# Optimization experiments

Measured on AMD Instinct MI355X. Metric: run time of the kernel, lower is better.

The kernel has to match this reference:

```python
import jax, jax.numpy as jnp
import numpy as np

B, N, FIN, FOUT, K, NNZ = 16, 50000, 32, 32, 6, 800000


def setup_inputs() -> dict:
    key = jax.random.key(0)
    k1, k2, k3, k4, k5 = jax.random.split(key, 5)
    x = jax.random.normal(k1, (B, N, FIN), dtype=jnp.float32)
    rows = jax.random.randint(k2, (NNZ,), 0, N, dtype=jnp.int32)
    cols = jax.random.randint(k3, (NNZ,), 0, N, dtype=jnp.int32)
    # values of the already-rescaled Laplacian (2L/lmax - I), scaled to keep the
    # Chebyshev recurrence numerically tame
    vals = jax.random.normal(k4, (NNZ,), dtype=jnp.float32) * 0.05
    W = jax.random.normal(k5, (FIN * K, FOUT), dtype=jnp.float32) * 0.02
    return {"x": x, "rows": rows, "cols": cols, "vals": vals, "W": W}


def reference(x, rows, cols, vals, W):
    # x: [B, N, Fin]
    def spmm(X):  # L @ X via gather + segment-sum scatter; X: [N, D]
        return jax.ops.segment_sum(vals[:, None] * X[cols], rows, num_segments=N)

    # [N, Fin, B] -> [N, Fin*B], matching the TF layout
    x0 = jnp.transpose(x, (1, 2, 0)).reshape(N, FIN * B)
    xs = [x0]
    x1 = spmm(x0)
    xs.append(x1)
    for _ in range(2, K):  # Chebyshev recurrence T_k = 2 L T_{k-1} - T_{k-2}
        x2 = 2.0 * spmm(x1) - x0
        xs.append(x2)
        x0, x1 = x1, x2
    Xk = jnp.stack(xs, axis=0)                       # [K, N, Fin*B]
    Xk = Xk.reshape(K, N, FIN, B)
    Xk = jnp.transpose(Xk, (3, 1, 2, 0))             # [B, N, Fin, K]
    Xk = Xk.reshape(B * N, FIN * K)
    out = Xk @ W                                      # [B*N, Fout]
    return out.reshape(B, N, FOUT)
```

## Files before the change

kernel.cpp:

```cpp
#include <hip/hip_runtime.h>
#include <hip/hip_bf16.h>

#define NND   50000
#define NBATCH 16
#define NFIN  32
#define NFOUT 32
#define NCHEB 6
#define NNZE  800000
#define DDIM  512

typedef __attribute__((ext_vector_type(8))) short    short8;
typedef __attribute__((ext_vector_type(8))) unsigned short u16x8;
typedef __attribute__((ext_vector_type(4))) float    f32x4;
typedef __attribute__((ext_vector_type(2))) float    f32x2;

__device__ __forceinline__ float b2f(unsigned short u) {
  union { unsigned u; float f; } v; v.u = ((unsigned)u) << 16; return v.f;
}
__device__ __forceinline__ unsigned short f2bf(float f) {
  union { float f; unsigned u; } v; v.f = f;
  unsigned r = v.u + 0x7fffu + ((v.u >> 16) & 1u);
  return (unsigned short)(r >> 16);
}
__device__ __forceinline__ unsigned f2fp8(float f) {
  unsigned s = (__float_as_uint(f) >> 24) & 0x80u;
  float af = fminf(fabsf(f), 448.0f);
  unsigned b;
  if (af < 0.015625f) {
    b = (unsigned)__float2int_rn(af * 512.0f);
  } else {
    unsigned u = __float_as_uint(af);
    u += 0x7FFFFu + ((u >> 20) & 1u);
    b = (((u >> 23) - 120u) << 3) | ((u >> 20) & 7u);
    if (b > 0x7Eu) b = 0x7Eu;
  }
  return s | b;
}

__global__ void hist_kernel(const int* __restrict__ rows, int* __restrict__ cnt, int nnz) {
  int e = blockIdx.x * blockDim.x + threadIdx.x;
  if (e < nnz) atomicAdd(&cnt[rows[e]], 1);
}

__global__ __launch_bounds__(1024) void scanA_kernel(const int* __restrict__ cnt,
                                                     int* __restrict__ rowptr,
                                                     int* __restrict__ partials, int n) {
  __shared__ int lds[1024];
  int b = blockIdx.x, tid = threadIdx.x, i = b * 1024 + tid;
  int v = (i < n) ? cnt[i] : 0;
  lds[tid] = v;
  __syncthreads();
  int s = v;
  for (int off = 1; off < 1024; off <<= 1) {
    int t = (tid >= off) ? lds[tid - off] : 0;
    __syncthreads();
    s += t;
    lds[tid] = s;
    __syncthreads();
  }
  if (i < n) rowptr[i] = s - v;
  if (tid == 1023) partials[b] = s;
}

__global__ void scanB_wprep(int* __restrict__ partials, int nb,
                            const float* __restrict__ W, unsigned short* __restrict__ Wfrag) {
  int t = threadIdx.x;
  if (t == 0) {
    int run = 0;
    for (int b = 0; b < nb; ++b) { int x = partials[b]; partials[b] = run; run += x; }
  } else if (t >= 64 && t < 64 + 768) {
    int w = t - 64;
    int frag = w >> 6, lane = w & 63;
    int kk = frag >> 1, h = frag & 1;
    int fo = (lane & 15) + h * 16, kc = (lane >> 4) * 8;
    u16x8 b;
#pragma unroll
    for (int j = 0; j < 8; ++j)
      b[j] = f2bf(W[((size_t)(kc + j) * NCHEB + kk) * NFOUT + fo]);
    *(u16x8*)(Wfrag + (size_t)w * 8) = b;
  }
}

__global__ __launch_bounds__(1024) void scanC_kernel(const int* __restrict__ partials,
                                                     int* __restrict__ rowptr,
                                                     int* __restrict__ cursor, int n) {
  int i = blockIdx.x * 1024 + threadIdx.x;
  if (i < n) {
    int r = rowptr[i] + partials[blockIdx.x];
    rowptr[i] = r;
    cursor[i] = r;
  }
  if (i == n) rowptr[n] = NNZE;
}

__global__ void fill_kernel(const int* __restrict__ rows, const int* __restrict__ cols,
                            const float* __restrict__ vals, int* __restrict__ cursor,
                            long* __restrict__ ecv, int nnz) {
  int e = blockIdx.x * blockDim.x + threadIdx.x;
  if (e < nnz) {
    int r = rows[e];
    int p = atomicAdd(&cursor[r], 1);
    ecv[p] = (long)((unsigned long long)__float_as_uint(vals[e]) << 32 | (unsigned)cols[e]);
  }
}

__global__ __launch_bounds__(256) void cheb_k0_q(const float* __restrict__ x,
                                                 unsigned short* __restrict__ T0,
                                                 char* __restrict__ Tq0) {
  int wave = threadIdx.x >> 6, lane = threadIdx.x & 63;
  int n = blockIdx.x * 4 + wave;
  int kc = (lane >> 4) * 8;
  int b  = lane & 15;

  const float* xp = x + ((size_t)b * NND + n) * NFIN + kc;
  float4 xa = *(const float4*)xp;
  float4 xb = *(const float4*)(xp + 4);
  float tv[8] = {xa.x, xa.y, xa.z, xa.w, xb.x, xb.y, xb.z, xb.w};

  u16x8 tb;
#pragma unroll
  for (int j = 0; j < 8; ++j) tb[j] = f2bf(tv[j]);
  *(u16x8*)(T0 + (size_t)n * DDIM + lane * 8) = tb;

  unsigned lo = f2fp8(tv[0]) | (f2fp8(tv[1]) << 8) | (f2fp8(tv[2]) << 16) | (f2fp8(tv[3]) << 24);
  unsigned hi = f2fp8(tv[4]) | (f2fp8(tv[5]) << 8) | (f2fp8(tv[6]) << 16) | (f2fp8(tv[7]) << 24);
  int2 qq; qq.x = (int)lo; qq.y = (int)hi;
  *(int2*)(Tq0 + (size_t)n * 512 + lane * 8) = qq;
}

__device__ __forceinline__ void gather_q(const char* __restrict__ qbase,
                                         const long* __restrict__ ecv,
                                         int s, int e1, float acc[8]) {
  int e = s;
  for (; e + 8 <= e1; e += 8) {
    long m[8];
#pragma unroll
    for (int q = 0; q < 8; ++q) m[q] = __builtin_nontemporal_load(ecv + e + q);
    int2 d[8];
#pragma unroll
    for (int q = 0; q < 8; ++q) d[q] = *(const int2*)(qbase + (size_t)(int)m[q] * 512);
#pragma unroll
    for (int q = 0; q < 8; ++q) {
      float v = __int_as_float((int)(m[q] >> 32));
      f32x2 f01 = __builtin_amdgcn_cvt_pk_f32_fp8(d[q].x, false);
      f32x2 f23 = __builtin_amdgcn_cvt_pk_f32_fp8(d[q].x, true);
      f32x2 f45 = __builtin_amdgcn_cvt_pk_f32_fp8(d[q].y, false);
      f32x2 f67 = __builtin_amdgcn_cvt_pk_f32_fp8(d[q].y, true);
      acc[0] = fmaf(v, f01.x, acc[0]);
      acc[1] = fmaf(v, f01.y, acc[1]);
      acc[2] = fmaf(v, f23.x, acc[2]);
      acc[3] = fmaf(v, f23.y, acc[3]);
      acc[4] = fmaf(v, f45.x, acc[4]);
      acc[5] = fmaf(v, f45.y, acc[5]);
      acc[6] = fmaf(v, f67.x, acc[6]);
      acc[7] = fmaf(v, f67.y, acc[7]);
    }
  }
  if (e + 4 <= e1) {
    long m[4];
#pragma unroll
    for (int q = 0; q < 4; ++q) m[q] = __builtin_nontemporal_load(ecv + e + q);
    int2 d[4];
#pragma unroll
    for (int q = 0; q < 4; ++q) d[q] = *(const int2*)(qbase + (size_t)(int)m[q] * 512);
#pragma unroll
    for (int q = 0; q < 4; ++q) {
      float v = __int_as_float((int)(m[q] >> 32));
      f32x2 f01 = __builtin_amdgcn_cvt_pk_f32_fp8(d[q].x, false);
      f32x2 f23 = __builtin_amdgcn_cvt_pk_f32_fp8(d[q].x, true);
      f32x2 f45 = __builtin_amdgcn_cvt_pk_f32_fp8(d[q].y, false);
      f32x2 f67 = __builtin_amdgcn_cvt_pk_f32_fp8(d[q].y, true);
      acc[0] = fmaf(v, f01.x, acc[0]);
      acc[1] = fmaf(v, f01.y, acc[1]);
      acc[2] = fmaf(v, f23.x, acc[2]);
      acc[3] = fmaf(v, f23.y, acc[3]);
      acc[4] = fmaf(v, f45.x, acc[4]);
      acc[5] = fmaf(v, f45.y, acc[5]);
      acc[6] = fmaf(v, f67.x, acc[6]);
      acc[7] = fmaf(v, f67.y, acc[7]);
    }
    e += 4;
  }
  for (; e < e1; ++e) {
    long mm = __builtin_nontemporal_load(ecv + e);
    int2 dd = *(const int2*)(qbase + (size_t)(int)mm * 512);
    float v = __int_as_float((int)(mm >> 32));
    f32x2 f01 = __builtin_amdgcn_cvt_pk_f32_fp8(dd.x, false);
    f32x2 f23 = __builtin_amdgcn_cvt_pk_f32_fp8(dd.x, true);
    f32x2 f45 = __builtin_amdgcn_cvt_pk_f32_fp8(dd.y, false);
    f32x2 f67 = __builtin_amdgcn_cvt_pk_f32_fp8(dd.y, true);
    acc[0] = fmaf(v, f01.x, acc[0]);
    acc[1] = fmaf(v, f01.y, acc[1]);
    acc[2] = fmaf(v, f23.x, acc[2]);
    acc[3] = fmaf(v, f23.y, acc[3]);
    acc[4] = fmaf(v, f45.x, acc[4]);
    acc[5] = fmaf(v, f45.y, acc[5]);
    acc[6] = fmaf(v, f67.x, acc[6]);
    acc[7] = fmaf(v, f67.y, acc[7]);
  }
}

__global__ __launch_bounds__(256) void cheb_level_q(const char* __restrict__ Tqprev,
                                                    const unsigned short* __restrict__ Tpp,
                                                    unsigned short* __restrict__ Tdst,
                                                    char* __restrict__ Tqdst,
                                                    const int* __restrict__ rowptr,
                                                    const long* __restrict__ ecv,
                                                    float alpha, float beta) {
  int wave = threadIdx.x >> 6, lane = threadIdx.x & 63;
  int n = blockIdx.x * 4 + wave;
  int s = rowptr[n], e1 = rowptr[n + 1];
  size_t rowoff = (size_t)n * DDIM + lane * 8;

  u16x8 tp2 = {};
  if (beta != 0.f) tp2 = *(const u16x8*)(Tpp + rowoff);

  float acc[8] = {0.f, 0.f, 0.f, 0.f, 0.f, 0.f, 0.f, 0.f};
  gather_q(Tqprev + (size_t)lane * 8, ecv, s, e1, acc);

  float tk[8];
  if (beta != 0.f) {
#pragma unroll
    for (int j = 0; j < 8; ++j) tk[j] = alpha * acc[j] - beta * b2f(tp2[j]);
  } else {
#pragma unroll
    for (int j = 0; j < 8; ++j) tk[j] = alpha * acc[j];
  }

  u16x8 tkb;
#pragma unroll
  for (int j = 0; j < 8; ++j) tkb[j] = f2bf(tk[j]);
  *(u16x8*)(Tdst + rowoff) = tkb;

  unsigned lo = f2fp8(tk[0]) | (f2fp8(tk[1]) << 8) | (f2fp8(tk[2]) << 16) | (f2fp8(tk[3]) << 24);
  unsigned hi = f2fp8(tk[4]) | (f2fp8(tk[5]) << 8) | (f2fp8(tk[6]) << 16) | (f2fp8(tk[7]) << 24);
  int2 qq; qq.x = (int)lo; qq.y = (int)hi;
  *(int2*)(Tqdst + (size_t)n * 512 + lane * 8) = qq;
}

__global__ __launch_bounds__(256) void cheb_level5_epi_q(const char* __restrict__ Tq4,
                                                         const unsigned short* __restrict__ Tall,
                                                         const unsigned short* __restrict__ Wfrag,
                                                         const int* __restrict__ rowptr,
                                                         const long* __restrict__ ecv,
                                                         float* __restrict__ out) {
  int wave = threadIdx.x >> 6, lane = threadIdx.x & 63;
  int n = blockIdx.x * 4 + wave;
  int s = rowptr[n], e1 = rowptr[n + 1];
  size_t rowoff = (size_t)n * DDIM + lane * 8;

  float acc[8] = {0.f, 0.f, 0.f, 0.f, 0.f, 0.f, 0.f, 0.f};
  gather_q(Tq4 + (size_t)lane * 8, ecv, s, e1, acc);

  short8 a[5];
#pragma unroll
  for (int kk = 0; kk < 5; ++kk)
    a[kk] = *(const short8*)(Tall + (size_t)kk * NND * DDIM + rowoff);

  u16x8 tp2 = __builtin_bit_cast(u16x8, a[3]);
  u16x8 t5b;
#pragma unroll
  for (int j = 0; j < 8; ++j) t5b[j] = f2bf(2.f * acc[j] - b2f(tp2[j]));

  int fo = lane & 15;
  f32x4 c0 = {0.f, 0.f, 0.f, 0.f}, c1 = {0.f, 0.f, 0.f, 0.f};
#pragma unroll
  for (int kk = 0; kk < 5; ++kk) {
    short8 B0 = *(const short8*)(Wfrag + ((size_t)(kk * 2 + 0) * 64 + lane) * 8);
    short8 B1 = *(const short8*)(Wfrag + ((size_t)(kk * 2 + 1) * 64 + lane) * 8);
    c0 = __builtin_amdgcn_mfma_f32_16x16x32_bf16(a[kk], B0, c0, 0, 0, 0);
    c1 = __builtin_amdgcn_mfma_f32_16x16x32_bf16(a[kk], B1, c1, 0, 0, 0);
  }
  {
    short8 a5 = __builtin_bit_cast(short8, t5b);
    short8 B0 = *(const short8*)(Wfrag + ((size_t)(5 * 2 + 0) * 64 + lane) * 8);
    short8 B1 = *(const short8*)(Wfrag + ((size_t)(5 * 2 + 1) * 64 + lane) * 8);
    c0 = __builtin_amdgcn_mfma_f32_16x16x32_bf16(a5, B0, c0, 0, 0, 0);
    c1 = __builtin_amdgcn_mfma_f32_16x16x32_bf16(a5, B1, c1, 0, 0, 0);
  }

  int br = (lane >> 4) * 4;
#pragma unroll
  for (int r = 0; r < 4; ++r) {
    size_t o = ((size_t)(br + r) * NND + n) * NFOUT + fo;
    out[o]      = c0[r];
    out[o + 16] = c1[r];
  }
}

__device__ __forceinline__ void gather_row(const unsigned short* __restrict__ gbase,
                                           const int* __restrict__ ccol,
                                           const float* __restrict__ cval,
                                           int s, int e1, float acc[8]) {
  int e = s;
  for (; e + 4 <= e1; e += 4) {
    int c[4]; float v[4];
#pragma unroll
    for (int q = 0; q < 4; ++q) {
      c[q] = __builtin_nontemporal_load(ccol + e + q);
      v[q] = __builtin_nontemporal_load(cval + e + q);
    }
    u16x8 t[4];
#pragma unroll
    for (int q = 0; q < 4; ++q) t[q] = *(const u16x8*)(gbase + (size_t)c[q] * DDIM);
#pragma unroll
    for (int q = 0; q < 4; ++q)
#pragma unroll
      for (int j = 0; j < 8; ++j) acc[j] = fmaf(v[q], b2f(t[q][j]), acc[j]);
  }
  for (; e < e1; ++e) {
    int   ci = __builtin_nontemporal_load(ccol + e);
    float vi = __builtin_nontemporal_load(cval + e);
    u16x8 ti = *(const u16x8*)(gbase + (size_t)ci * DDIM);
#pragma unroll
    for (int j = 0; j < 8; ++j) acc[j] = fmaf(vi, b2f(ti[j]), acc[j]);
  }
}

__global__ void scan_kernel(const int* __restrict__ cnt, int* __restrict__ rowptr,
                            int* __restrict__ cursor, int n) {
  __shared__ int lds[1024];
  int tid = threadIdx.x;
  int run = 0;
  for (int base = 0; base <= n; base += 1024) {
    int i = base + tid;
    int v = (i < n) ? cnt[i] : 0;
    lds[tid] = v;
    __syncthreads();
    int s = v;
    for (int off = 1; off < 1024; off <<= 1) {
      int t = (tid >= off) ? lds[tid - off] : 0;
      __syncthreads();
      s += t;
      lds[tid] = s;
      __syncthreads();
    }
    int excl = run + s - v;
    if (i <= n) {
      rowptr[i] = excl;
      if (i < n) cursor[i] = excl;
    }
    run += lds[1023];
    __syncthreads();
  }
}

__global__ void fill2_kernel(const int* __restrict__ rows, const int* __restrict__ cols,
                             const float* __restrict__ vals, int* __restrict__ cursor,
                             int* __restrict__ ccol, float* __restrict__ cval, int nnz) {
  int e = blockIdx.x * blockDim.x + threadIdx.x;
  if (e < nnz) {
    int r = rows[e];
    int p = atomicAdd(&cursor[r], 1);
    ccol[p] = cols[e];
    cval[p] = vals[e];
  }
}

__global__ __launch_bounds__(256) void cheb_k0_fused(const float* __restrict__ x,
                                                     unsigned short* __restrict__ T0,
                                                     const float* __restrict__ W,
                                                     float* __restrict__ out) {
  int wave = threadIdx.x >> 6, lane = threadIdx.x & 63;
  int n = blockIdx.x * 4 + wave;
  int fo = lane & 15, kc = (lane >> 4) * 8;
  int b  = lane & 15;

  const float* xp = x + ((size_t)b * NND + n) * NFIN + kc;
  float4 xa = *(const float4*)xp;
  float4 xb = *(const float4*)(xp + 4);
  float tv[8] = {xa.x, xa.y, xa.z, xa.w, xb.x, xb.y, xb.z, xb.w};

  u16x8 tb;
#pragma unroll
  for (int j = 0; j < 8; ++j) tb[j] = f2bf(tv[j]);
  *(u16x8*)(T0 + (size_t)n * DDIM + lane * 8) = tb;

  short8 B0, B1;
#pragma unroll
  for (int j = 0; j < 8; ++j) {
    int fi = kc + j;
    const float* wp = W + ((size_t)fi * NCHEB + 0) * NFOUT + fo;
    B0[j] = (short)f2bf(wp[0]);
    B1[j] = (short)f2bf(wp[16]);
  }
  f32x4 c0 = {0.f, 0.f, 0.f, 0.f}, c1 = {0.f, 0.f, 0.f, 0.f};
  short8 a = __builtin_bit_cast(short8, tb);
  c0 = __builtin_amdgcn_mfma_f32_16x16x32_bf16(a, B0, c0, 0, 0, 0);
  c1 = __builtin_amdgcn_mfma_f32_16x16x32_bf16(a, B1, c1, 0, 0, 0);

  int br = (lane >> 4) * 4;
#pragma unroll
  for (int r = 0; r < 4; ++r) {
    size_t o = ((size_t)(br + r) * NND + n) * NFOUT + fo;
    out[o]      = c0[r];
    out[o + 16] = c1[r];
  }
}

__global__ __launch_bounds__(256) void cheb_level_fused(const unsigned short* __restrict__ Tprev,
                                                        unsigned short* __restrict__ Tio,
                                                        const int* __restrict__ rowptr,
                                                        const int* __restrict__ ccol,
                                                        const float* __restrict__ cval,
                                                        const float* __restrict__ W,
                                                        float* __restrict__ out,
                                                        int kk, float alpha, float beta, int writeT) {
  int wave = threadIdx.x >> 6, lane = threadIdx.x & 63;
  int n = blockIdx.x * 4 + wave;
  int fo = lane & 15, kc = (lane >> 4) * 8;

  short8 B0, B1;
#pragma unroll
  for (int j = 0; j < 8; ++j) {
    int fi = kc + j;
    const float* wp = W + ((size_t)fi * NCHEB + kk) * NFOUT + fo;
    B0[j] = (short)f2bf(wp[0]);
    B1[j] = (short)f2bf(wp[16]);
  }

  float acc[8] = {0.f, 0.f, 0.f, 0.f, 0.f, 0.f, 0.f, 0.f};
  int s = rowptr[n], e1 = rowptr[n + 1];
  gather_row(Tprev + lane * 8, ccol, cval, s, e1, acc);

  unsigned short* iop = Tio + (size_t)n * DDIM + lane * 8;
  float tk[8];
  if (beta != 0.f) {
    u16x8 tp2 = *(const u16x8*)iop;
#pragma unroll
    for (int j = 0; j < 8; ++j) tk[j] = alpha * acc[j] - beta * b2f(tp2[j]);
  } else {
#pragma unroll
    for (int j = 0; j < 8; ++j) tk[j] = alpha * acc[j];
  }

  u16x8 tkb;
#pragma unroll
  for (int j = 0; j < 8; ++j) tkb[j] = f2bf(tk[j]);
  if (writeT) *(u16x8*)iop = tkb;

  f32x4 c0 = {0.f, 0.f, 0.f, 0.f}, c1 = {0.f, 0.f, 0.f, 0.f};
  short8 a = __builtin_bit_cast(short8, tkb);
  c0 = __builtin_amdgcn_mfma_f32_16x16x32_bf16(a, B0, c0, 0, 0, 0);
  c1 = __builtin_amdgcn_mfma_f32_16x16x32_bf16(a, B1, c1, 0, 0, 0);

  int br = (lane >> 4) * 4;
#pragma unroll
  for (int r = 0; r < 4; ++r) {
    size_t o = ((size_t)(br + r) * NND + n) * NFOUT + fo;
    out[o]      += c0[r];
    out[o + 16] += c1[r];
  }
}

static inline size_t alignup(size_t v) { return (v + 255) & ~(size_t)255; }

extern "C" void kernel_launch(void* const* d_in, const int* in_sizes, int n_in,
                              void* d_out, int out_size, void* d_ws, size_t ws_size,
                              hipStream_t stream) {
  const float* x    = (const float*)d_in[0];
  const int*   rows = (const int*)d_in[1];
  const int*   cols = (const int*)d_in[2];
  const float* vals = (const float*)d_in[3];
  const float* W    = (const float*)d_in[4];
  float* out = (float*)d_out;

  const size_t tbytes = alignup((size_t)NND * DDIM * 2);
  const size_t qbytes = alignup((size_t)NND * 512);
  const size_t small  = alignup((size_t)(NND + 1) * 4);
  const size_t need_q = 5 * tbytes + 2 * qbytes + alignup(12 * 64 * 8 * 2)
                      + 4 * small + alignup((size_t)NNZE * 8);

  const int grid  = NND / 4;
  const int nscan = (NND + 1023) / 1024;

  if (ws_size >= need_q) {
    char* p = (char*)d_ws;
    size_t off = 0;
    unsigned short* Tall  = (unsigned short*)(p + off); off += 5 * tbytes;
    char* bufQA = (char*)(p + off); off += qbytes;
    char* bufQB = (char*)(p + off); off += qbytes;
    unsigned short* Wfrag = (unsigned short*)(p + off); off += alignup(12 * 64 * 8 * 2);
    int*  cnt      = (int*)(p + off); off += small;
    int*  rowptr   = (int*)(p + off); off += small;
    int*  cursor   = (int*)(p + off); off += small;
    int*  partials = (int*)(p + off); off += small;
    long* ecv      = (long*)(p + off); off += alignup((size_t)NNZE * 8);

    hipMemsetAsync(cnt, 0, (size_t)NND * 4, stream);
    hist_kernel<<<(NNZE + 255) / 256, 256, 0, stream>>>(rows, cnt, NNZE);
    scanA_kernel<<<nscan, 1024, 0, stream>>>(cnt, rowptr, partials, NND);
    scanB_wprep<<<1, 832, 0, stream>>>(partials, nscan, W, Wfrag);
    scanC_kernel<<<nscan, 1024, 0, stream>>>(partials, rowptr, cursor, NND);
    fill_kernel<<<(NNZE + 255) / 256, 256, 0, stream>>>(rows, cols, vals, cursor, ecv, NNZE);

    auto Tk = [&](int k) { return Tall + (size_t)k * NND * DDIM; };

    cheb_k0_q<<<grid, 256, 0, stream>>>(x, Tk(0), bufQA);
    cheb_level_q<<<grid, 256, 0, stream>>>(bufQA, nullptr, Tk(1), bufQB, rowptr, ecv, 1.f, 0.f);
    cheb_level_q<<<grid, 256, 0, stream>>>(bufQB, Tk(0), Tk(2), bufQA, rowptr, ecv, 2.f, 1.f);
    cheb_level_q<<<grid, 256, 0, stream>>>(bufQA, Tk(1), Tk(3), bufQB, rowptr, ecv, 2.f, 1.f);
    cheb_level_q<<<grid, 256, 0, stream>>>(bufQB, Tk(2), Tk(4), bufQA, rowptr, ecv, 2.f, 1.f);
    cheb_level5_epi_q<<<grid, 256, 0, stream>>>(bufQA, Tall, Wfrag, rowptr, ecv, out);
  } else {
    char* p = (char*)d_ws;
    size_t off = 0;
    unsigned short* bufA = (unsigned short*)(p + off); off += tbytes;
    unsigned short* bufB = (unsigned short*)(p + off); off += tbytes;
    int*   cnt    = (int*)(p + off); off += small;
    int*   rowptr = (int*)(p + off); off += small;
    int*   cursor = (int*)(p + off); off += small;
    int*   ccol   = (int*)(p + off); off += alignup((size_t)NNZE * 4);
    float* cval   = (float*)(p + off); off += alignup((size_t)NNZE * 4);

    hipMemsetAsync(cnt, 0, (size_t)NND * 4, stream);
    hist_kernel<<<(NNZE + 255) / 256, 256, 0, stream>>>(rows, cnt, NNZE);
    scan_kernel<<<1, 1024, 0, stream>>>(cnt, rowptr, cursor, NND);
    fill2_kernel<<<(NNZE + 255) / 256, 256, 0, stream>>>(rows, cols, vals, cursor, ccol, cval, NNZE);

    cheb_k0_fused<<<grid, 256, 0, stream>>>(x, bufA, W, out);
    cheb_level_fused<<<grid, 256, 0, stream>>>(bufA, bufB, rowptr, ccol, cval, W, out, 1, 1.f, 0.f, 1);
    cheb_level_fused<<<grid, 256, 0, stream>>>(bufB, bufA, rowptr, ccol, cval, W, out, 2, 2.f, 1.f, 1);
    cheb_level_fused<<<grid, 256, 0, stream>>>(bufA, bufB, rowptr, ccol, cval, W, out, 3, 2.f, 1.f, 1);
    cheb_level_fused<<<grid, 256, 0, stream>>>(bufB, bufA, rowptr, ccol, cval, W, out, 4, 2.f, 1.f, 1);
    cheb_level_fused<<<grid, 256, 0, stream>>>(bufA, bufB, rowptr, ccol, cval, W, out, 5, 2.f, 1.f, 0);
  }
}
```

Baseline: 552.5 us.

## Slice feature dimension into 8 node-major planes for cache-local SpMM gathers

```diff
diff --git a/kernel.cpp b/kernel.cpp
--- a/kernel.cpp
+++ b/kernel.cpp
@@ -8,8 +8,10 @@
 #define NCHEB 6
 #define NNZE  800000
 #define DDIM  512
+#define NSLICE 8
 
 typedef __attribute__((ext_vector_type(8))) short    short8;
+typedef __attribute__((ext_vector_type(4))) short    short4v;
 typedef __attribute__((ext_vector_type(8))) unsigned short u16x8;
 typedef __attribute__((ext_vector_type(4))) float    f32x4;
 typedef __attribute__((ext_vector_type(2))) float    f32x2;
@@ -104,48 +106,132 @@
   }
 }
 
-__global__ __launch_bounds__(256) void cheb_k0_q(const float* __restrict__ x,
-                                                 unsigned short* __restrict__ T0,
-                                                 char* __restrict__ Tq0) {
+
+__global__ __launch_bounds__(256) void cheb_k0_slice(const float* __restrict__ x,
+                                                     unsigned short* __restrict__ Tb0,
+                                                     char* __restrict__ Tq0) {
   int wave = threadIdx.x >> 6, lane = threadIdx.x & 63;
   int n = blockIdx.x * 4 + wave;
-  int kc = (lane >> 4) * 8;
-  int b  = lane & 15;
-
-  const float* xp = x + ((size_t)b * NND + n) * NFIN + kc;
+  int bb = lane & 15, kc = (lane >> 4) * 8;
+  int sA = kc >> 2;
+
+  const float* xp = x + ((size_t)bb * NND + n) * NFIN + kc;
   float4 xa = *(const float4*)xp;
   float4 xb = *(const float4*)(xp + 4);
   float tv[8] = {xa.x, xa.y, xa.z, xa.w, xb.x, xb.y, xb.z, xb.w};
 
-  u16x8 tb;
-#pragma unroll
-  for (int j = 0; j < 8; ++j) tb[j] = f2bf(tv[j]);
-  *(u16x8*)(T0 + (size_t)n * DDIM + lane * 8) = tb;
-
-  unsigned lo = f2fp8(tv[0]) | (f2fp8(tv[1]) << 8) | (f2fp8(tv[2]) << 16) | (f2fp8(tv[3]) << 24);
-  unsigned hi = f2fp8(tv[4]) | (f2fp8(tv[5]) << 8) | (f2fp8(tv[6]) << 16) | (f2fp8(tv[7]) << 24);
-  int2 qq; qq.x = (int)lo; qq.y = (int)hi;
-  *(int2*)(Tq0 + (size_t)n * 512 + lane * 8) = qq;
-}
-
-__device__ __forceinline__ void gather_q(const char* __restrict__ qbase,
-                                         const long* __restrict__ ecv,
-                                         int s, int e1, float acc[8]) {
-  int e = s;
+  size_t roA = ((size_t)sA * NND + n) * 64 + 4 * bb;
+  size_t roB = roA + (size_t)NND * 64;
+
+  short4v lo, hi;
+#pragma unroll
+  for (int j = 0; j < 4; ++j) { lo[j] = (short)f2bf(tv[j]); hi[j] = (short)f2bf(tv[4 + j]); }
+  *(short4v*)(Tb0 + roA) = lo;
+  *(short4v*)(Tb0 + roB) = hi;
+
+  unsigned qlo = f2fp8(tv[0]) | (f2fp8(tv[1]) << 8) | (f2fp8(tv[2]) << 16) | (f2fp8(tv[3]) << 24);
+  unsigned qhi = f2fp8(tv[4]) | (f2fp8(tv[5]) << 8) | (f2fp8(tv[6]) << 16) | (f2fp8(tv[7]) << 24);
+  *(int*)(Tq0 + roA) = (int)qlo;
+  *(int*)(Tq0 + roB) = (int)qhi;
+}
+
+__global__ __launch_bounds__(256) void cheb_level_slice(const char* __restrict__ Tqprev,
+                                                        const unsigned short* __restrict__ TppB,
+                                                        unsigned short* __restrict__ TdstB,
+                                                        char* __restrict__ TdstQ,
+                                                        const int* __restrict__ rowptr,
+                                                        const long* __restrict__ ecv,
+                                                        float alpha, float beta) {
+  int s    = blockIdx.x & 7;
+  int blk  = blockIdx.x >> 3;
+  int wave = threadIdx.x >> 6, lane = threadIdx.x & 63;
+  int g = lane >> 4, fl = lane & 15;
+  int n = blk * 16 + wave * 4 + g;
+
+  int s0 = rowptr[n], deg = rowptr[n + 1] - s0;
+  const char* qsrc = Tqprev + (size_t)s * ((size_t)NND * 64) + 4 * fl;
+
+  float acc[4] = {0.f, 0.f, 0.f, 0.f};
+  for (int i = 0; i < deg; i += 8) {
+    int cols[8]; float vals[8];
+#pragma unroll
+    for (int q = 0; q < 8; ++q) {
+      int idx = (i + q < deg) ? (i + q) : (deg - 1);
+      long m = __builtin_nontemporal_load(ecv + s0 + idx);
+      cols[q] = (int)(unsigned)m;
+      vals[q] = (i + q < deg) ? __int_as_float((int)(m >> 32)) : 0.f;
+    }
+    int d[8];
+#pragma unroll
+    for (int q = 0; q < 8; ++q) d[q] = *(const int*)(qsrc + (size_t)cols[q] * 64);
+#pragma unroll
+    for (int q = 0; q < 8; ++q) {
+      f32x2 f01 = __builtin_amdgcn_cvt_pk_f32_fp8(d[q], false);
+      f32x2 f23 = __builtin_amdgcn_cvt_pk_f32_fp8(d[q], true);
+      acc[0] = fmaf(vals[q], f01.x, acc[0]);
+      acc[1] = fmaf(vals[q], f01.y, acc[1]);
+      acc[2] = fmaf(vals[q], f23.x, acc[2]);
+      acc[3] = fmaf(vals[q], f23.y, acc[3]);
+    }
+  }
+
+  size_t ro = ((size_t)s * NND + n) * 64 + 4 * fl;
+  float tk[4];
+  if (beta != 0.f) {
+    short4v tb = *(const short4v*)(TppB + ro);
+#pragma unroll
+    for (int j = 0; j < 4; ++j) tk[j] = alpha * acc[j] - beta * b2f((unsigned short)tb[j]);
+  } else {
+#pragma unroll
+    for (int j = 0; j < 4; ++j) tk[j] = alpha * acc[j];
+  }
+
+  short4v o;
+#pragma unroll
+  for (int j = 0; j < 4; ++j) o[j] = (short)f2bf(tk[j]);
+  __builtin_nontemporal_store(o, (short4v*)(TdstB + ro));
+
+  unsigned w = f2fp8(tk[0]) | (f2fp8(tk[1]) << 8) | (f2fp8(tk[2]) << 16) | (f2fp8(tk[3]) << 24);
+  *(int*)(TdstQ + ro) = (int)w;
+}
+
+__global__ __launch_bounds__(256) void cheb_l5_epi_slice(const char* __restrict__ Tq4,
+                                                         const unsigned short* __restrict__ Tall,
+                                                         const unsigned short* __restrict__ Wfrag,
+                                                         const int* __restrict__ rowptr,
+                                                         const long* __restrict__ ecv,
+                                                         float* __restrict__ out) {
+  int wave = threadIdx.x >> 6, lane = threadIdx.x & 63;
+  int n = blockIdx.x * 4 + wave;
+  int bb = lane & 15, kc = (lane >> 4) * 8;
+  int sA = kc >> 2;
+  size_t roA = ((size_t)sA * NND + n) * 64 + 4 * bb;
+  size_t roB = roA + (size_t)NND * 64;
+
+  int s0 = rowptr[n], e1 = rowptr[n + 1];
+  const char* qlo = Tq4 + (size_t)sA * ((size_t)NND * 64) + 4 * bb;
+  const char* qhi = qlo + (size_t)NND * 64;
+
+  float acc[8] = {0.f, 0.f, 0.f, 0.f, 0.f, 0.f, 0.f, 0.f};
+  int e = s0;
   for (; e + 8 <= e1; e += 8) {
     long m[8];
 #pragma unroll
     for (int q = 0; q < 8; ++q) m[q] = __builtin_nontemporal_load(ecv + e + q);
-    int2 d[8];
-#pragma unroll
-    for (int q = 0; q < 8; ++q) d[q] = *(const int2*)(qbase + (size_t)(int)m[q] * 512);
+    int dlo[8], dhi[8];
+#pragma unroll
+    for (int q = 0; q < 8; ++q) {
+      size_t co = (size_t)(unsigned)m[q] * 64;
+      dlo[q] = *(const int*)(qlo + co);
+      dhi[q] = *(const int*)(qhi + co);
+    }
 #pragma unroll
     for (int q = 0; q < 8; ++q) {
       float v = __int_as_float((int)(m[q] >> 32));
-      f32x2 f01 = __builtin_amdgcn_cvt_pk_f32_fp8(d[q].x, false);
-      f32x2 f23 = __builtin_amdgcn_cvt_pk_f32_fp8(d[q].x, true);
-      f32x2 f45 = __builtin_amdgcn_cvt_pk_f32_fp8(d[q].y, false);
-      f32x2 f67 = __builtin_amdgcn_cvt_pk_f32_fp8(d[q].y, true);
+      f32x2 f01 = __builtin_amdgcn_cvt_pk_f32_fp8(dlo[q], false);
+      f32x2 f23 = __builtin_amdgcn_cvt_pk_f32_fp8(dlo[q], true);
+      f32x2 f45 = __builtin_amdgcn_cvt_pk_f32_fp8(dhi[q], false);
+      f32x2 f67 = __builtin_amdgcn_cvt_pk_f32_fp8(dhi[q], true);
       acc[0] = fmaf(v, f01.x, acc[0]);
       acc[1] = fmaf(v, f01.y, acc[1]);
       acc[2] = fmaf(v, f23.x, acc[2]);
@@ -156,39 +242,16 @@
       acc[7] = fmaf(v, f67.y, acc[7]);
     }
   }
-  if (e + 4 <= e1) {
-    long m[4];
-#pragma unroll
-    for (int q = 0; q < 4; ++q) m[q] = __builtin_nontemporal_load(ecv + e + q);
-    int2 d[4];
-#pragma unroll
-    for (int q = 0; q < 4; ++q) d[q] = *(const int2*)(qbase + (size_t)(int)m[q] * 512);
-#pragma unroll
-    for (int q = 0; q < 4; ++q) {
-      float v = __int_as_float((int)(m[q] >> 32));
-      f32x2 f01 = __builtin_amdgcn_cvt_pk_f32_fp8(d[q].x, false);
-      f32x2 f23 = __builtin_amdgcn_cvt_pk_f32_fp8(d[q].x, true);
-      f32x2 f45 = __builtin_amdgcn_cvt_pk_f32_fp8(d[q].y, false);
-      f32x2 f67 = __builtin_amdgcn_cvt_pk_f32_fp8(d[q].y, true);
-      acc[0] = fmaf(v, f01.x, acc[0]);
-      acc[1] = fmaf(v, f01.y, acc[1]);
-      acc[2] = fmaf(v, f23.x, acc[2]);
-      acc[3] = fmaf(v, f23.y, acc[3]);
-      acc[4] = fmaf(v, f45.x, acc[4]);
-      acc[5] = fmaf(v, f45.y, acc[5]);
-      acc[6] = fmaf(v, f67.x, acc[6]);
-      acc[7] = fmaf(v, f67.y, acc[7]);
-    }
-    e += 4;
-  }
   for (; e < e1; ++e) {
     long mm = __builtin_nontemporal_load(ecv + e);
-    int2 dd = *(const int2*)(qbase + (size_t)(int)mm * 512);
+    size_t co = (size_t)(unsigned)mm * 64;
+    int dl = *(const int*)(qlo + co);
+    int dh = *(const int*)(qhi + co);
     float v = __int_as_float((int)(mm >> 32));
-    f32x2 f01 = __builtin_amdgcn_cvt_pk_f32_fp8(dd.x, false);
-    f32x2 f23 = __builtin_amdgcn_cvt_pk_f32_fp8(dd.x, true);
-    f32x2 f45 = __builtin_amdgcn_cvt_pk_f32_fp8(dd.y, false);
-    f32x2 f67 = __builtin_amdgcn_cvt_pk_f32_fp8(dd.y, true);
+    f32x2 f01 = __builtin_amdgcn_cvt_pk_f32_fp8(dl, false);
+    f32x2 f23 = __builtin_amdgcn_cvt_pk_f32_fp8(dl, true);
+    f32x2 f45 = __builtin_amdgcn_cvt_pk_f32_fp8(dh, false);
+    f32x2 f67 = __builtin_amdgcn_cvt_pk_f32_fp8(dh, true);
     acc[0] = fmaf(v, f01.x, acc[0]);
     acc[1] = fmaf(v, f01.y, acc[1]);
     acc[2] = fmaf(v, f23.x, acc[2]);
@@ -198,85 +261,32 @@
     acc[6] = fmaf(v, f67.x, acc[6]);
     acc[7] = fmaf(v, f67.y, acc[7]);
   }
-}
-
-__global__ __launch_bounds__(256) void cheb_level_q(const char* __restrict__ Tqprev,
-                                                    const unsigned short* __restrict__ Tpp,
-                                                    unsigned short* __restrict__ Tdst,
-                                                    char* __restrict__ Tqdst,
-                                                    const int* __restrict__ rowptr,
-                                                    const long* __restrict__ ecv,
-                                                    float alpha, float beta) {
-  int wave = threadIdx.x >> 6, lane = threadIdx.x & 63;
-  int n = blockIdx.x * 4 + wave;
-  int s = rowptr[n], e1 = rowptr[n + 1];
-  size_t rowoff = (size_t)n * DDIM + lane * 8;
-
-  u16x8 tp2 = {};
-  if (beta != 0.f) tp2 = *(const u16x8*)(Tpp + rowoff);
-
-  float acc[8] = {0.f, 0.f, 0.f, 0.f, 0.f, 0.f, 0.f, 0.f};
-  gather_q(Tqprev + (size_t)lane * 8, ecv, s, e1, acc);
-
-  float tk[8];
-  if (beta != 0.f) {
-#pragma unroll
-    for (int j = 0; j < 8; ++j) tk[j] = alpha * acc[j] - beta * b2f(tp2[j]);
-  } else {
-#pragma unroll
-    for (int j = 0; j < 8; ++j) tk[j] = alpha * acc[j];
-  }
-
-  u16x8 tkb;
-#pragma unroll
-  for (int j = 0; j < 8; ++j) tkb[j] = f2bf(tk[j]);
-  *(u16x8*)(Tdst + rowoff) = tkb;
-
-  unsigned lo = f2fp8(tk[0]) | (f2fp8(tk[1]) << 8) | (f2fp8(tk[2]) << 16) | (f2fp8(tk[3]) << 24);
-  unsigned hi = f2fp8(tk[4]) | (f2fp8(tk[5]) << 8) | (f2fp8(tk[6]) << 16) | (f2fp8(tk[7]) << 24);
-  int2 qq; qq.x = (int)lo; qq.y = (int)hi;
-  *(int2*)(Tqdst + (size_t)n * 512 + lane * 8) = qq;
-}
-
-__global__ __launch_bounds__(256) void cheb_level5_epi_q(const char* __restrict__ Tq4,
-                                                         const unsigned short* __restrict__ Tall,
-                                                         const unsigned short* __restrict__ Wfrag,
-                                                         const int* __restrict__ rowptr,
-                                                         const long* __restrict__ ecv,
-                                                         float* __restrict__ out) {
-  int wave = threadIdx.x >> 6, lane = threadIdx.x & 63;
-  int n = blockIdx.x * 4 + wave;
-  int s = rowptr[n], e1 = rowptr[n + 1];
-  size_t rowoff = (size_t)n * DDIM + lane * 8;
-
-  float acc[8] = {0.f, 0.f, 0.f, 0.f, 0.f, 0.f, 0.f, 0.f};
-  gather_q(Tq4 + (size_t)lane * 8, ecv, s, e1, acc);
-
-  short8 a[5];
-#pragma unroll
-  for (int kk = 0; kk < 5; ++kk)
-    a[kk] = *(const short8*)(Tall + (size_t)kk * NND * DDIM + rowoff);
+
+  short8 a[6];
+#pragma unroll
+  for (int kk = 0; kk < 5; ++kk) {
+    short4v lo = *(const short4v*)(Tall + (size_t)kk * NND * DDIM + roA);
+    short4v hi = *(const short4v*)(Tall + (size_t)kk * NND * DDIM + roB);
+    short8 r;
+    r[0]=lo[0]; r[1]=lo[1]; r[2]=lo[2]; r[3]=lo[3];
+    r[4]=hi[0]; r[5]=hi[1]; r[6]=hi[2]; r[7]=hi[3];
+    a[kk] = r;
+  }
 
   u16x8 tp2 = __builtin_bit_cast(u16x8, a[3]);
   u16x8 t5b;
 #pragma unroll
   for (int j = 0; j < 8; ++j) t5b[j] = f2bf(2.f * acc[j] - b2f(tp2[j]));
+  a[5] = __builtin_bit_cast(short8, t5b);
 
   int fo = lane & 15;
   f32x4 c0 = {0.f, 0.f, 0.f, 0.f}, c1 = {0.f, 0.f, 0.f, 0.f};
 #pragma unroll
-  for (int kk = 0; kk < 5; ++kk) {
+  for (int kk = 0; kk < 6; ++kk) {
     short8 B0 = *(const short8*)(Wfrag + ((size_t)(kk * 2 + 0) * 64 + lane) * 8);
     short8 B1 = *(const short8*)(Wfrag + ((size_t)(kk * 2 + 1) * 64 + lane) * 8);
     c0 = __builtin_amdgcn_mfma_f32_16x16x32_bf16(a[kk], B0, c0, 0, 0, 0);
     c1 = __builtin_amdgcn_mfma_f32_16x16x32_bf16(a[kk], B1, c1, 0, 0, 0);
-  }
-  {
-    short8 a5 = __builtin_bit_cast(short8, t5b);
-    short8 B0 = *(const short8*)(Wfrag + ((size_t)(5 * 2 + 0) * 64 + lane) * 8);
-    short8 B1 = *(const short8*)(Wfrag + ((size_t)(5 * 2 + 1) * 64 + lane) * 8);
-    c0 = __builtin_amdgcn_mfma_f32_16x16x32_bf16(a5, B0, c0, 0, 0, 0);
-    c1 = __builtin_amdgcn_mfma_f32_16x16x32_bf16(a5, B1, c1, 0, 0, 0);
   }
 
   int br = (lane >> 4) * 4;
@@ -468,18 +478,19 @@
   const size_t tbytes = alignup((size_t)NND * DDIM * 2);
   const size_t qbytes = alignup((size_t)NND * 512);
   const size_t small  = alignup((size_t)(NND + 1) * 4);
-  const size_t need_q = 5 * tbytes + 2 * qbytes + alignup(12 * 64 * 8 * 2)
+  const size_t need_s = 5 * tbytes + 2 * qbytes + alignup(12 * 64 * 8 * 2)
                       + 4 * small + alignup((size_t)NNZE * 8);
 
   const int grid  = NND / 4;
+  const int sgrid = (NND / 16) * NSLICE;
   const int nscan = (NND + 1023) / 1024;
 
-  if (ws_size >= need_q) {
+  if (ws_size >= need_s) {
     char* p = (char*)d_ws;
     size_t off = 0;
-    unsigned short* Tall  = (unsigned short*)(p + off); off += 5 * tbytes;
-    char* bufQA = (char*)(p + off); off += qbytes;
-    char* bufQB = (char*)(p + off); off += qbytes;
+    unsigned short* Tall = (unsigned short*)(p + off); off += 5 * tbytes;
+    char* TqA = (char*)(p + off); off += qbytes;
+    char* TqB = (char*)(p + off); off += qbytes;
     unsigned short* Wfrag = (unsigned short*)(p + off); off += alignup(12 * 64 * 8 * 2);
     int*  cnt      = (int*)(p + off); off += small;
     int*  rowptr   = (int*)(p + off); off += small;
@@ -496,12 +507,12 @@
 
     auto Tk = [&](int k) { return Tall + (size_t)k * NND * DDIM; };
 
-    cheb_k0_q<<<grid, 256, 0, stream>>>(x, Tk(0), bufQA);
-    cheb_level_q<<<grid, 256, 0, stream>>>(bufQA, nullptr, Tk(1), bufQB, rowptr, ecv, 1.f, 0.f);
-    cheb_level_q<<<grid, 256, 0, stream>>>(bufQB, Tk(0), Tk(2), bufQA, rowptr, ecv, 2.f, 1.f);
-    cheb_level_q<<<grid, 256, 0, stream>>>(bufQA, Tk(1), Tk(3), bufQB, rowptr, ecv, 2.f, 1.f);
-    cheb_level_q<<<grid, 256, 0, stream>>>(bufQB, Tk(2), Tk(4), bufQA, rowptr, ecv, 2.f, 1.f);
-    cheb_level5_epi_q<<<grid, 256, 0, stream>>>(bufQA, Tall, Wfrag, rowptr, ecv, out);
+    cheb_k0_slice<<<grid, 256, 0, stream>>>(x, Tk(0), TqA);
+    cheb_level_slice<<<sgrid, 256, 0, stream>>>(TqA, nullptr, Tk(1), TqB, rowptr, ecv, 1.f, 0.f);
+    cheb_level_slice<<<sgrid, 256, 0, stream>>>(TqB, Tk(0), Tk(2), TqA, rowptr, ecv, 2.f, 1.f);
+    cheb_level_slice<<<sgrid, 256, 0, stream>>>(TqA, Tk(1), Tk(3), TqB, rowptr, ecv, 2.f, 1.f);
+    cheb_level_slice<<<sgrid, 256, 0, stream>>>(TqB, Tk(2), Tk(4), TqA, rowptr, ecv, 2.f, 1.f);
+    cheb_l5_epi_slice<<<grid, 256, 0, stream>>>(TqA, Tall, Wfrag, rowptr, ecv, out);
   } else {
     char* p = (char*)d_ws;
     size_t off = 0;
```

Result: slower. 942.4 us (+70.6%).
